# Kernel optimization log

Measured on AMD Instinct MI355X. Metric: run time of the kernel, lower is better.

Reference implementation:

```python
import jax, jax.numpy as jnp
import numpy as np

N_NODES = 50000
N_EDGES = 800000
D_FEAT = 64
IN_DIM = 1 + 2 * D_FEAT  # 129
FC_DIMS = [128, 64, 1]


def setup_inputs() -> dict:
    key = jax.random.key(0)
    ks = jax.random.split(key, 10)
    x = jax.random.normal(ks[0], (N_NODES, D_FEAT), dtype=jnp.float32)
    edge_index = jax.random.randint(ks[1], (2, N_EDGES), 0, N_NODES, dtype=jnp.int64)
    edge_weight = jax.random.uniform(ks[2], (N_EDGES, 1), dtype=jnp.float32)
    # MLP params (Linear: y = x @ W.T + b), Kaiming-ish scale
    dims = [IN_DIM] + FC_DIMS
    W1 = jax.random.normal(ks[3], (dims[1], dims[0]), dtype=jnp.float32) / np.sqrt(dims[0])
    b1 = jnp.zeros((dims[1],), dtype=jnp.float32)
    W2 = jax.random.normal(ks[4], (dims[2], dims[1]), dtype=jnp.float32) / np.sqrt(dims[1])
    b2 = jnp.zeros((dims[2],), dtype=jnp.float32)
    W3 = jax.random.normal(ks[5], (dims[3], dims[2]), dtype=jnp.float32) / np.sqrt(dims[2])
    b3 = jnp.zeros((dims[3],), dtype=jnp.float32)
    return {"x": x, "edge_index": edge_index, "edge_weight": edge_weight,
            "W1": W1, "b1": b1, "W2": W2, "b2": b2, "W3": W3, "b3": b3}


def reference(x, edge_index, edge_weight, W1, b1, W2, b2, W3, b3):
    # Gather source/target node features per edge: [E, d]
    src = x[edge_index[0]]
    tgt = x[edge_index[1]]
    # Concat [edge_weight | src | tgt] -> [E, 1 + 2d]
    h = jnp.concatenate([edge_weight, src, tgt], axis=1)
    # MLP (dropout is None / eval; last layer dim==1 -> no ReLU)
    h = jax.nn.relu(h @ W1.T + b1)
    h = jax.nn.relu(h @ W2.T + b2)
    return h @ W3.T + b3  # [E, 1] new edge weights
```

## Files before the change

### kernel.cpp

```cpp
#include <hip/hip_runtime.h>

typedef _Float16 half8 __attribute__((ext_vector_type(8)));
typedef _Float16 half4_t __attribute__((ext_vector_type(4)));
typedef float floatx4 __attribute__((ext_vector_type(4)));

#define LP 136

__global__ __launch_bounds__(256) void prep_kernel(
    const float* __restrict__ x,
    const float* __restrict__ W1, const float* __restrict__ W2,
    _Float16* __restrict__ wsh, _Float16* __restrict__ xh, int n_x8)
{
    int b = blockIdx.x;
    if (b < 96) {
        int tid = b * 256 + threadIdx.x;
        if (tid < 16384) {
            int c = tid >> 9, r = tid & 511;
            int L = r >> 3, jj = r & 7;
            int mt = c >> 2, kb = c & 3;
            int n = mt * 16 + (L & 15);
            int k = kb * 32 + (L >> 4) * 8 + jj;
            wsh[tid] = (_Float16)W1[n * 129 + 1 + k];
        } else {
            int t = tid - 16384;
            int c = t >> 9, r = t & 511;
            int L = r >> 3, jj = r & 7;
            int mt = c >> 2, kb = c & 3;
            int i = mt * 16 + (L & 15);
            int j = kb * 32 + (L >> 4) * 8 + jj;
            wsh[tid] = (_Float16)W2[i * 128 + j];
        }
    } else {
        int t2 = (b - 96) * 256 + threadIdx.x;
        if (t2 < n_x8) {
            const float4* p = (const float4*)(x + (size_t)t2 * 8);
            float4 v0 = p[0], v1 = p[1];
            half8 h = {(_Float16)v0.x, (_Float16)v0.y, (_Float16)v0.z, (_Float16)v0.w,
                       (_Float16)v1.x, (_Float16)v1.y, (_Float16)v1.z, (_Float16)v1.w};
            *(half8*)(xh + (size_t)t2 * 8) = h;
        }
    }
}

__global__ __launch_bounds__(256, 4) void edge_mlp_kernel(
    const _Float16* __restrict__ xh,
    const int* __restrict__ ei,
    const float* __restrict__ ew,
    const float* __restrict__ W1, const float* __restrict__ b1,
    const float* __restrict__ b2,
    const float* __restrict__ W3, const float* __restrict__ b3,
    const _Float16* __restrict__ wf,
    float* __restrict__ out, int E)
{
    __shared__ __align__(16) _Float16 hA[128 * LP];
    __shared__ float s_b1[128];
    __shared__ float s_c0[128];
    __shared__ float s_b2[64];
    __shared__ float s_w3[64];

    const int tid = threadIdx.x;
    const int e_blk = blockIdx.x * 128;
    const int lane = tid & 63;
    const int wave = tid >> 6;
    const int lrow = lane & 15;
    const int quad = lane >> 4;

    if (tid < 128) {
        s_b1[tid] = b1[tid];
        s_c0[tid] = W1[tid * 129];
    } else if (tid < 192) {
        int i = tid - 128;
        s_b2[i] = b2[i];
        s_w3[i] = W3[i];
    }

    {
        int e_loc = wave * 32 + (lane >> 1);
        int part = lane & 1;
        int e = e_blk + e_loc; if (e >= E) e = E - 1;
        int node = ei[(size_t)part * E + e];
        const _Float16* rp = xh + (size_t)node * 64;
        _Float16* dst = &hA[e_loc * LP + part * 64];
#pragma unroll
        for (int q = 0; q < 8; ++q)
            *(half8*)(dst + q * 8) = *(const half8*)(rp + q * 8);
    }
    __syncthreads();

    float ewv[2];
#pragma unroll
    for (int et = 0; et < 2; ++et) {
        int e = e_blk + wave * 32 + et * 16 + lrow;
        if (e >= E) e = E - 1;
        ewv[et] = ew[e];
    }

    half8 bfr[2][4];
#pragma unroll
    for (int et = 0; et < 2; ++et)
#pragma unroll
        for (int kb = 0; kb < 4; ++kb)
            bfr[et][kb] = *(const half8*)(&hA[(wave * 32 + et * 16 + lrow) * LP + kb * 32 + quad * 8]);

#pragma unroll
    for (int mt = 0; mt < 8; ++mt) {
        half8 afr[4];
#pragma unroll
        for (int kb = 0; kb < 4; ++kb)
            afr[kb] = *(const half8*)(wf + (mt * 4 + kb) * 512 + lane * 8);
        floatx4 bb = *(const floatx4*)(&s_b1[mt * 16 + quad * 4]);
        floatx4 cc = *(const floatx4*)(&s_c0[mt * 16 + quad * 4]);
#pragma unroll
        for (int et = 0; et < 2; ++et) {
            floatx4 a = {0.f, 0.f, 0.f, 0.f};
#pragma unroll
            for (int kb = 0; kb < 4; ++kb)
                a = __builtin_amdgcn_mfma_f32_16x16x32_f16(afr[kb], bfr[et][kb], a, 0, 0, 0);
            half4_t hv;
#pragma unroll
            for (int r = 0; r < 4; ++r)
                hv[r] = (_Float16)fmaxf(a[r] + bb[r] + ewv[et] * cc[r], 0.f);
            *(half4_t*)(&hA[(wave * 32 + et * 16 + lrow) * LP + mt * 16 + quad * 4]) = hv;
        }
    }

    half8 b2fr[2][4];
#pragma unroll
    for (int et = 0; et < 2; ++et)
#pragma unroll
        for (int kb = 0; kb < 4; ++kb)
            b2fr[et][kb] = *(const half8*)(&hA[(wave * 32 + et * 16 + lrow) * LP + kb * 32 + quad * 8]);

    float p[2] = {0.f, 0.f};
#pragma unroll
    for (int mt = 0; mt < 4; ++mt) {
        half8 afr[4];
#pragma unroll
        for (int kb = 0; kb < 4; ++kb)
            afr[kb] = *(const half8*)(wf + 16384 + (mt * 4 + kb) * 512 + lane * 8);
        floatx4 bb = *(const floatx4*)(&s_b2[mt * 16 + quad * 4]);
        floatx4 ww = *(const floatx4*)(&s_w3[mt * 16 + quad * 4]);
#pragma unroll
        for (int et = 0; et < 2; ++et) {
            floatx4 a = {0.f, 0.f, 0.f, 0.f};
#pragma unroll
            for (int kb = 0; kb < 4; ++kb)
                a = __builtin_amdgcn_mfma_f32_16x16x32_f16(afr[kb], b2fr[et][kb], a, 0, 0, 0);
#pragma unroll
            for (int r = 0; r < 4; ++r)
                p[et] += fmaxf(a[r] + bb[r], 0.f) * ww[r];
        }
    }
#pragma unroll
    for (int et = 0; et < 2; ++et) {
        p[et] += __shfl_xor(p[et], 16, 64);
        p[et] += __shfl_xor(p[et], 32, 64);
    }
    float b3v = b3[0];
    if (quad < 2) {
        int oe = e_blk + wave * 32 + quad * 16 + lrow;
        if (oe < E) out[oe] = b3v + p[quad];
    }
}

extern "C" void kernel_launch(void* const* d_in, const int* in_sizes, int n_in,
                              void* d_out, int out_size, void* d_ws, size_t ws_size,
                              hipStream_t stream) {
    const float* x  = (const float*)d_in[0];
    const int*   ei = (const int*)d_in[1];
    const float* ew = (const float*)d_in[2];
    const float* W1 = (const float*)d_in[3];
    const float* b1 = (const float*)d_in[4];
    const float* W2 = (const float*)d_in[5];
    const float* b2 = (const float*)d_in[6];
    const float* W3 = (const float*)d_in[7];
    const float* b3 = (const float*)d_in[8];
    float* out = (float*)d_out;
    const int E = in_sizes[2];
    const int n_x = in_sizes[0];
    const int n_x8 = n_x / 8;

    _Float16* wsh = (_Float16*)d_ws;
    _Float16* xh  = (_Float16*)((char*)d_ws + 49152);

    int xblk = (n_x8 + 255) / 256;
    prep_kernel<<<96 + xblk, 256, 0, stream>>>(x, W1, W2, wsh, xh, n_x8);

    int nblk = (E + 127) / 128;
    edge_mlp_kernel<<<nblk, 256, 0, stream>>>(xh, ei, ew, W1, b1, b2, W3, b3,
                                              wsh, out, E);
}
```

Baseline: 150.1 us.

## Make edge MLP persistent with register-resident weights and prefetched gathers

Replaces the one-block-per-128-edges kernel with a persistent grid of 512 blocks in which each wave loops over 16-edge tiles. All W1/W2 fragments and biases are loaded into registers once per wave, and the next tile's node-feature gather goes straight into MFMA operand registers while the current tile computes. This removes the block-wide shared-memory staging, the __syncthreads, and the repeated weight reloads per tile. The cost is heavy register pressure (launch bounds lowered to 1 block per SM), lower occupancy, and reliance on one tile of software prefetch to hide gather latency.

```diff
diff --git a/kernel.cpp b/kernel.cpp
--- a/kernel.cpp
+++ b/kernel.cpp
@@ -4,12 +4,13 @@
 typedef _Float16 half4_t __attribute__((ext_vector_type(4)));
 typedef float floatx4 __attribute__((ext_vector_type(4)));
 
-#define LP 136
+#define H1P 136
 
 __global__ __launch_bounds__(256) void prep_kernel(
     const float* __restrict__ x,
     const float* __restrict__ W1, const float* __restrict__ W2,
-    _Float16* __restrict__ wsh, _Float16* __restrict__ xh, int n_x8)
+    _Float16* __restrict__ wsh, float* __restrict__ c0f,
+    _Float16* __restrict__ xh, int n_x8)
 {
     int b = blockIdx.x;
     if (b < 96) {
@@ -30,8 +31,10 @@
             int j = kb * 32 + (L >> 4) * 8 + jj;
             wsh[tid] = (_Float16)W2[i * 128 + j];
         }
+    } else if (b == 96) {
+        if (threadIdx.x < 128) c0f[threadIdx.x] = W1[threadIdx.x * 129];
     } else {
-        int t2 = (b - 96) * 256 + threadIdx.x;
+        int t2 = (b - 97) * 256 + threadIdx.x;
         if (t2 < n_x8) {
             const float4* p = (const float4*)(x + (size_t)t2 * 8);
             float4 v0 = p[0], v1 = p[1];
@@ -42,124 +45,123 @@
     }
 }
 
-__global__ __launch_bounds__(256, 4) void edge_mlp_kernel(
+__global__ __launch_bounds__(256, 1) void edge_mlp_kernel(
     const _Float16* __restrict__ xh,
     const int* __restrict__ ei,
     const float* __restrict__ ew,
-    const float* __restrict__ W1, const float* __restrict__ b1,
+    const float* __restrict__ b1, const float* __restrict__ c0f,
     const float* __restrict__ b2,
     const float* __restrict__ W3, const float* __restrict__ b3,
     const _Float16* __restrict__ wf,
-    float* __restrict__ out, int E)
+    float* __restrict__ out, int E, int NT, int NW)
 {
-    __shared__ __align__(16) _Float16 hA[128 * LP];
-    __shared__ float s_b1[128];
-    __shared__ float s_c0[128];
-    __shared__ float s_b2[64];
-    __shared__ float s_w3[64];
+    __shared__ __align__(16) _Float16 h1s[4][16 * H1P];
 
     const int tid = threadIdx.x;
-    const int e_blk = blockIdx.x * 128;
     const int lane = tid & 63;
     const int wave = tid >> 6;
     const int lrow = lane & 15;
     const int quad = lane >> 4;
 
-    if (tid < 128) {
-        s_b1[tid] = b1[tid];
-        s_c0[tid] = W1[tid * 129];
-    } else if (tid < 192) {
-        int i = tid - 128;
-        s_b2[i] = b2[i];
-        s_w3[i] = W3[i];
+    half8 w1f[8][4], w2f[4][4];
+#pragma unroll
+    for (int mt = 0; mt < 8; ++mt)
+#pragma unroll
+        for (int kb = 0; kb < 4; ++kb)
+            w1f[mt][kb] = *(const half8*)(wf + (mt * 4 + kb) * 512 + lane * 8);
+#pragma unroll
+    for (int mt = 0; mt < 4; ++mt)
+#pragma unroll
+        for (int kb = 0; kb < 4; ++kb)
+            w2f[mt][kb] = *(const half8*)(wf + 16384 + (mt * 4 + kb) * 512 + lane * 8);
+
+    floatx4 b1v[8], c0v[8], b2v[4], w3v[4];
+#pragma unroll
+    for (int mt = 0; mt < 8; ++mt) {
+        b1v[mt] = *(const floatx4*)(b1 + mt * 16 + quad * 4);
+        c0v[mt] = *(const floatx4*)(c0f + mt * 16 + quad * 4);
+    }
+#pragma unroll
+    for (int mt = 0; mt < 4; ++mt) {
+        b2v[mt] = *(const floatx4*)(b2 + mt * 16 + quad * 4);
+        w3v[mt] = *(const floatx4*)(W3 + mt * 16 + quad * 4);
+    }
+    const float b3v = b3[0];
+
+    _Float16* h1p = &h1s[wave][0];
+
+    int t = blockIdx.x * 4 + wave;
+    if (t >= NT) return;
+
+    half8 cb[4]; float cew;
+    {
+        int e = t * 16 + lrow; if (e >= E) e = E - 1;
+        int ns = ei[e], ntg = ei[E + e];
+        const _Float16* ps = xh + (size_t)ns * 64;
+        const _Float16* pt = xh + (size_t)ntg * 64;
+        cb[0] = *(const half8*)(ps + quad * 8);
+        cb[1] = *(const half8*)(ps + 32 + quad * 8);
+        cb[2] = *(const half8*)(pt + quad * 8);
+        cb[3] = *(const half8*)(pt + 32 + quad * 8);
+        cew = ew[e];
     }
 
-    {
-        int e_loc = wave * 32 + (lane >> 1);
-        int part = lane & 1;
-        int e = e_blk + e_loc; if (e >= E) e = E - 1;
-        int node = ei[(size_t)part * E + e];
-        const _Float16* rp = xh + (size_t)node * 64;
-        _Float16* dst = &hA[e_loc * LP + part * 64];
-#pragma unroll
-        for (int q = 0; q < 8; ++q)
-            *(half8*)(dst + q * 8) = *(const half8*)(rp + q * 8);
-    }
-    __syncthreads();
-
-    float ewv[2];
-#pragma unroll
-    for (int et = 0; et < 2; ++et) {
-        int e = e_blk + wave * 32 + et * 16 + lrow;
-        if (e >= E) e = E - 1;
-        ewv[et] = ew[e];
-    }
-
-    half8 bfr[2][4];
-#pragma unroll
-    for (int et = 0; et < 2; ++et)
-#pragma unroll
-        for (int kb = 0; kb < 4; ++kb)
-            bfr[et][kb] = *(const half8*)(&hA[(wave * 32 + et * 16 + lrow) * LP + kb * 32 + quad * 8]);
+    while (t < NT) {
+        const int tn = t + NW;
+        half8 nb[4]; float new_;
+        {
+            int tt = (tn < NT) ? tn : t;
+            int e2 = tt * 16 + lrow; if (e2 >= E) e2 = E - 1;
+            int ns = ei[e2], ntg = ei[E + e2];
+            const _Float16* ps = xh + (size_t)ns * 64;
+            const _Float16* pt = xh + (size_t)ntg * 64;
+            nb[0] = *(const half8*)(ps + quad * 8);
+            nb[1] = *(const half8*)(ps + 32 + quad * 8);
+            nb[2] = *(const half8*)(pt + quad * 8);
+            nb[3] = *(const half8*)(pt + 32 + quad * 8);
+            new_ = ew[e2];
+        }
 
 #pragma unroll
-    for (int mt = 0; mt < 8; ++mt) {
-        half8 afr[4];
+        for (int mt = 0; mt < 8; ++mt) {
+            floatx4 a;
 #pragma unroll
-        for (int kb = 0; kb < 4; ++kb)
-            afr[kb] = *(const half8*)(wf + (mt * 4 + kb) * 512 + lane * 8);
-        floatx4 bb = *(const floatx4*)(&s_b1[mt * 16 + quad * 4]);
-        floatx4 cc = *(const floatx4*)(&s_c0[mt * 16 + quad * 4]);
-#pragma unroll
-        for (int et = 0; et < 2; ++et) {
-            floatx4 a = {0.f, 0.f, 0.f, 0.f};
+            for (int r = 0; r < 4; ++r)
+                a[r] = b1v[mt][r] + cew * c0v[mt][r];
 #pragma unroll
             for (int kb = 0; kb < 4; ++kb)
-                a = __builtin_amdgcn_mfma_f32_16x16x32_f16(afr[kb], bfr[et][kb], a, 0, 0, 0);
+                a = __builtin_amdgcn_mfma_f32_16x16x32_f16(w1f[mt][kb], cb[kb], a, 0, 0, 0);
             half4_t hv;
 #pragma unroll
             for (int r = 0; r < 4; ++r)
-                hv[r] = (_Float16)fmaxf(a[r] + bb[r] + ewv[et] * cc[r], 0.f);
-            *(half4_t*)(&hA[(wave * 32 + et * 16 + lrow) * LP + mt * 16 + quad * 4]) = hv;
+                hv[r] = (_Float16)fmaxf(a[r], 0.f);
+            *(half4_t*)(h1p + lrow * H1P + mt * 16 + quad * 4) = hv;
         }
-    }
 
-    half8 b2fr[2][4];
-#pragma unroll
-    for (int et = 0; et < 2; ++et)
+        half8 hb[4];
 #pragma unroll
         for (int kb = 0; kb < 4; ++kb)
-            b2fr[et][kb] = *(const half8*)(&hA[(wave * 32 + et * 16 + lrow) * LP + kb * 32 + quad * 8]);
+            hb[kb] = *(const half8*)(h1p + lrow * H1P + kb * 32 + quad * 8);
 
-    float p[2] = {0.f, 0.f};
+        float p = 0.f;
 #pragma unroll
-    for (int mt = 0; mt < 4; ++mt) {
-        half8 afr[4];
-#pragma unroll
-        for (int kb = 0; kb < 4; ++kb)
-            afr[kb] = *(const half8*)(wf + 16384 + (mt * 4 + kb) * 512 + lane * 8);
-        floatx4 bb = *(const floatx4*)(&s_b2[mt * 16 + quad * 4]);
-        floatx4 ww = *(const floatx4*)(&s_w3[mt * 16 + quad * 4]);
-#pragma unroll
-        for (int et = 0; et < 2; ++et) {
-            floatx4 a = {0.f, 0.f, 0.f, 0.f};
+        for (int mt = 0; mt < 4; ++mt) {
+            floatx4 a = b2v[mt];
 #pragma unroll
             for (int kb = 0; kb < 4; ++kb)
-                a = __builtin_amdgcn_mfma_f32_16x16x32_f16(afr[kb], b2fr[et][kb], a, 0, 0, 0);
+                a = __builtin_amdgcn_mfma_f32_16x16x32_f16(w2f[mt][kb], hb[kb], a, 0, 0, 0);
 #pragma unroll
             for (int r = 0; r < 4; ++r)
-                p[et] += fmaxf(a[r] + bb[r], 0.f) * ww[r];
+                p += fmaxf(a[r], 0.f) * w3v[mt][r];
         }
-    }
-#pragma unroll
-    for (int et = 0; et < 2; ++et) {
-        p[et] += __shfl_xor(p[et], 16, 64);
-        p[et] += __shfl_xor(p[et], 32, 64);
-    }
-    float b3v = b3[0];
-    if (quad < 2) {
-        int oe = e_blk + wave * 32 + quad * 16 + lrow;
-        if (oe < E) out[oe] = b3v + p[quad];
+        p += __shfl_xor(p, 16, 64);
+        p += __shfl_xor(p, 32, 64);
+        int oe = t * 16 + lrow;
+        if (quad == 0 && oe < E) out[oe] = p + b3v;
+
+        t = tn;
+        cb[0] = nb[0]; cb[1] = nb[1]; cb[2] = nb[2]; cb[3] = nb[3];
+        cew = new_;
     }
 }
 
@@ -181,12 +183,15 @@
     const int n_x8 = n_x / 8;
 
     _Float16* wsh = (_Float16*)d_ws;
-    _Float16* xh  = (_Float16*)((char*)d_ws + 49152);
+    float*    c0f = (float*)((char*)d_ws + 49152);
+    _Float16* xh  = (_Float16*)((char*)d_ws + 51200);
 
     int xblk = (n_x8 + 255) / 256;
-    prep_kernel<<<96 + xblk, 256, 0, stream>>>(x, W1, W2, wsh, xh, n_x8);
+    prep_kernel<<<97 + xblk, 256, 0, stream>>>(x, W1, W2, wsh, c0f, xh, n_x8);
 
-    int nblk = (E + 127) / 128;
-    edge_mlp_kernel<<<nblk, 256, 0, stream>>>(xh, ei, ew, W1, b1, b2, W3, b3,
-                                              wsh, out, E);
+    const int NT = (E + 15) / 16;
+    const int GRID = 512;
+    const int NW = GRID * 4;
+    edge_mlp_kernel<<<GRID, 256, 0, stream>>>(xh, ei, ew, b1, c0f, b2, W3, b3,
+                                              wsh, out, E, NT, NW);
 }
```

Measured after the change: 178.2 us. 18.7% more time.

## Split edge MLP work across waves by output-neuron and edge halves

Applied to the files above, without the earlier changes.

Each wave now computes a 64-neuron by 64-edge tile (4x4 MFMA tiles) instead of all neurons for 32 edges. Each wave then loads only half of the W1/W2 fragments from global memory per k-block and reuses them across four edge tiles, which raises MFMA reuse per load. The cost is larger accumulator register use, extra block-wide barriers around the in-place hA overwrite, and a shared-memory reduction of the two partial layer-3 sums.

```diff
diff --git a/kernel.cpp b/kernel.cpp
--- a/kernel.cpp
+++ b/kernel.cpp
@@ -57,11 +57,14 @@
     __shared__ float s_c0[128];
     __shared__ float s_b2[64];
     __shared__ float s_w3[64];
+    __shared__ float s_out[2][128];
 
     const int tid = threadIdx.x;
     const int e_blk = blockIdx.x * 128;
     const int lane = tid & 63;
     const int wave = tid >> 6;
+    const int ns = wave >> 1;
+    const int es = wave & 1;
     const int lrow = lane & 15;
     const int quad = lane >> 4;
 
@@ -75,8 +78,8 @@
     }
 
     {
-        int e_loc = wave * 32 + (lane >> 1);
-        int part = lane & 1;
+        int e_loc = tid >> 1;
+        int part = tid & 1;
         int e = e_blk + e_loc; if (e >= E) e = E - 1;
         int node = ei[(size_t)part * E + e];
         const _Float16* rp = xh + (size_t)node * 64;
@@ -85,81 +88,107 @@
         for (int q = 0; q < 8; ++q)
             *(half8*)(dst + q * 8) = *(const half8*)(rp + q * 8);
     }
-    __syncthreads();
-
-    float ewv[2];
-#pragma unroll
-    for (int et = 0; et < 2; ++et) {
-        int e = e_blk + wave * 32 + et * 16 + lrow;
+
+    float ewv[4];
+#pragma unroll
+    for (int et = 0; et < 4; ++et) {
+        int e = e_blk + es * 64 + et * 16 + lrow;
         if (e >= E) e = E - 1;
         ewv[et] = ew[e];
     }
-
-    half8 bfr[2][4];
-#pragma unroll
-    for (int et = 0; et < 2; ++et)
-#pragma unroll
-        for (int kb = 0; kb < 4; ++kb)
-            bfr[et][kb] = *(const half8*)(&hA[(wave * 32 + et * 16 + lrow) * LP + kb * 32 + quad * 8]);
-
-#pragma unroll
-    for (int mt = 0; mt < 8; ++mt) {
-        half8 afr[4];
-#pragma unroll
-        for (int kb = 0; kb < 4; ++kb)
-            afr[kb] = *(const half8*)(wf + (mt * 4 + kb) * 512 + lane * 8);
-        floatx4 bb = *(const floatx4*)(&s_b1[mt * 16 + quad * 4]);
-        floatx4 cc = *(const floatx4*)(&s_c0[mt * 16 + quad * 4]);
-#pragma unroll
-        for (int et = 0; et < 2; ++et) {
-            floatx4 a = {0.f, 0.f, 0.f, 0.f};
-#pragma unroll
-            for (int kb = 0; kb < 4; ++kb)
-                a = __builtin_amdgcn_mfma_f32_16x16x32_f16(afr[kb], bfr[et][kb], a, 0, 0, 0);
+    __syncthreads();
+
+    floatx4 acc[4][4];
+#pragma unroll
+    for (int mt = 0; mt < 4; ++mt)
+#pragma unroll
+        for (int et = 0; et < 4; ++et)
+            acc[mt][et] = (floatx4){0.f, 0.f, 0.f, 0.f};
+
+#pragma unroll
+    for (int kb = 0; kb < 4; ++kb) {
+        half8 afr[4], bfr[4];
+#pragma unroll
+        for (int mt = 0; mt < 4; ++mt)
+            afr[mt] = *(const half8*)(wf + (size_t)(((4 * ns + mt) * 4 + kb) * 512 + lane * 8));
+#pragma unroll
+        for (int et = 0; et < 4; ++et)
+            bfr[et] = *(const half8*)(&hA[(es * 64 + et * 16 + lrow) * LP + kb * 32 + quad * 8]);
+#pragma unroll
+        for (int mt = 0; mt < 4; ++mt)
+#pragma unroll
+            for (int et = 0; et < 4; ++et)
+                acc[mt][et] = __builtin_amdgcn_mfma_f32_16x16x32_f16(afr[mt], bfr[et], acc[mt][et], 0, 0, 0);
+    }
+    __syncthreads();
+
+#pragma unroll
+    for (int mt = 0; mt < 4; ++mt) {
+        int nb = (4 * ns + mt) * 16 + quad * 4;
+        floatx4 bb = *(const floatx4*)(&s_b1[nb]);
+        floatx4 cc = *(const floatx4*)(&s_c0[nb]);
+#pragma unroll
+        for (int et = 0; et < 4; ++et) {
             half4_t hv;
 #pragma unroll
             for (int r = 0; r < 4; ++r)
-                hv[r] = (_Float16)fmaxf(a[r] + bb[r] + ewv[et] * cc[r], 0.f);
-            *(half4_t*)(&hA[(wave * 32 + et * 16 + lrow) * LP + mt * 16 + quad * 4]) = hv;
+                hv[r] = (_Float16)fmaxf(acc[mt][et][r] + bb[r] + ewv[et] * cc[r], 0.f);
+            *(half4_t*)(&hA[(es * 64 + et * 16 + lrow) * LP + nb]) = hv;
         }
     }
-
-    half8 b2fr[2][4];
-#pragma unroll
-    for (int et = 0; et < 2; ++et)
-#pragma unroll
-        for (int kb = 0; kb < 4; ++kb)
-            b2fr[et][kb] = *(const half8*)(&hA[(wave * 32 + et * 16 + lrow) * LP + kb * 32 + quad * 8]);
-
-    float p[2] = {0.f, 0.f};
-#pragma unroll
-    for (int mt = 0; mt < 4; ++mt) {
-        half8 afr[4];
-#pragma unroll
-        for (int kb = 0; kb < 4; ++kb)
-            afr[kb] = *(const half8*)(wf + 16384 + (mt * 4 + kb) * 512 + lane * 8);
-        floatx4 bb = *(const floatx4*)(&s_b2[mt * 16 + quad * 4]);
-        floatx4 ww = *(const floatx4*)(&s_w3[mt * 16 + quad * 4]);
-#pragma unroll
-        for (int et = 0; et < 2; ++et) {
-            floatx4 a = {0.f, 0.f, 0.f, 0.f};
-#pragma unroll
-            for (int kb = 0; kb < 4; ++kb)
-                a = __builtin_amdgcn_mfma_f32_16x16x32_f16(afr[kb], b2fr[et][kb], a, 0, 0, 0);
+    __syncthreads();
+
+    floatx4 acc2[2][4];
+#pragma unroll
+    for (int it = 0; it < 2; ++it)
+#pragma unroll
+        for (int et = 0; et < 4; ++et)
+            acc2[it][et] = (floatx4){0.f, 0.f, 0.f, 0.f};
+
+#pragma unroll
+    for (int kb = 0; kb < 4; ++kb) {
+        half8 a2[2], hb[4];
+#pragma unroll
+        for (int it = 0; it < 2; ++it)
+            a2[it] = *(const half8*)(wf + (size_t)(16384 + ((2 * ns + it) * 4 + kb) * 512 + lane * 8));
+#pragma unroll
+        for (int et = 0; et < 4; ++et)
+            hb[et] = *(const half8*)(&hA[(es * 64 + et * 16 + lrow) * LP + kb * 32 + quad * 8]);
+#pragma unroll
+        for (int it = 0; it < 2; ++it)
+#pragma unroll
+            for (int et = 0; et < 4; ++et)
+                acc2[it][et] = __builtin_amdgcn_mfma_f32_16x16x32_f16(a2[it], hb[et], acc2[it][et], 0, 0, 0);
+    }
+
+    float p[4] = {0.f, 0.f, 0.f, 0.f};
+#pragma unroll
+    for (int it = 0; it < 2; ++it) {
+        int ib = (2 * ns + it) * 16 + quad * 4;
+        floatx4 bb = *(const floatx4*)(&s_b2[ib]);
+        floatx4 ww = *(const floatx4*)(&s_w3[ib]);
+#pragma unroll
+        for (int et = 0; et < 4; ++et)
 #pragma unroll
             for (int r = 0; r < 4; ++r)
-                p[et] += fmaxf(a[r] + bb[r], 0.f) * ww[r];
-        }
-    }
-#pragma unroll
-    for (int et = 0; et < 2; ++et) {
+                p[et] += fmaxf(acc2[it][et][r] + bb[r], 0.f) * ww[r];
+    }
+#pragma unroll
+    for (int et = 0; et < 4; ++et) {
         p[et] += __shfl_xor(p[et], 16, 64);
         p[et] += __shfl_xor(p[et], 32, 64);
     }
-    float b3v = b3[0];
-    if (quad < 2) {
-        int oe = e_blk + wave * 32 + quad * 16 + lrow;
-        if (oe < E) out[oe] = b3v + p[quad];
+    if (quad == 0) {
+#pragma unroll
+        for (int et = 0; et < 4; ++et)
+            s_out[ns][es * 64 + et * 16 + lrow] = p[et];
+    }
+    __syncthreads();
+
+    if (tid < 128) {
+        int oe = e_blk + tid;
+        if (oe < E)
+            out[oe] = b3[0] + s_out[0][tid] + s_out[1][tid];
     }
 }
 
```

Result: faster. 147.0 us (-2.1%).
